# Performance work log

Measured on AMD Instinct MI355X. Metric: run time of the kernel, lower is better.

## Reference

```python
import jax, jax.numpy as jnp
import numpy as np

N, T, K, R = 192, 32, 3, 2  # nodes, timesteps, filter taps, downsampling rate


def setup_inputs() -> dict:
    key = jax.random.key(0)
    ks = jax.random.split(key, 7)
    X = jax.random.normal(ks[0], (N, T), dtype=jnp.float32)
    # scale Sg so powers of the product-graph shift stay numerically tame
    Sg = jax.random.normal(ks[1], (N, N), dtype=jnp.float32) / np.float32(np.sqrt(N))
    s = jax.random.normal(ks[2], (2, 2), dtype=jnp.float32) * 0.5
    h_e1 = jax.random.normal(ks[3], (16, 1, K), dtype=jnp.float32) * 0.3
    h_e2 = jax.random.normal(ks[4], (32, 16, K), dtype=jnp.float32) * 0.3
    h_d1 = jax.random.normal(ks[5], (16, 32, K), dtype=jnp.float32) * 0.3
    h_d2 = jax.random.normal(ks[6], (1, 16, K), dtype=jnp.float32) * 0.3
    return {"X": X, "Sg": Sg, "s": s, "h_e1": h_e1, "h_e2": h_e2,
            "h_d1": h_d1, "h_d2": h_d2}


def _temp_graph(t):
    # torch.eye(t).roll(1, dims=-1).t() : cyclic directed shift, S[(i+1)%t, i] = 1
    return jnp.roll(jnp.eye(t, dtype=jnp.float32), 1, axis=1).T


def _product_powers(St, Sg, s):
    # S = sum_{i,j in {0,1}} s[i,j] * kron(St^i, Sg^j); return stacked S^0..S^{K-1}
    t, n = St.shape[0], Sg.shape[0]
    It = jnp.eye(t, dtype=jnp.float32)
    In = jnp.eye(n, dtype=jnp.float32)
    S = (s[0, 0] * jnp.kron(It, In) + s[0, 1] * jnp.kron(It, Sg)
         + s[1, 0] * jnp.kron(St, In) + s[1, 1] * jnp.kron(St, Sg))
    powers = [jnp.eye(t * n, dtype=jnp.float32)]
    for _ in range(K - 1):
        powers.append(powers[-1] @ S)
    return jnp.stack(powers)  # (K, t*n, t*n)


def _conv(x, Sp, h):
    # GTConvLayerDense: Y[:, o] = sum_i sum_k h[o,i,k] * S^k @ x[:, i]
    xp = jnp.einsum('knm,mi->kni', Sp, x)  # (K, NT, Cin)
    return jnp.einsum('kni,oik->no', xp, h)  # (NT, Cout)


def _down(x, n, t):
    # columnvec layout: row index = time*n + node; max-pool over R consecutive times
    c = x.shape[-1]
    return x.reshape(t // R, R, n, c).max(axis=1).reshape((t // R) * n, c)


def _up(x, n, t, tt):
    # zero-stuff every R-th timestep up to target length tt
    c = x.shape[-1]
    z = jnp.zeros((tt, n, c), dtype=x.dtype)
    return z.at[::R].set(x.reshape(t, n, c)).reshape(tt * n, c)


def reference(X, Sg, s, h_e1, h_e2, h_d1, h_d2):
    n, t = X.shape
    Ts = [t, t // R, t // (R * R)]  # [32, 16, 8]
    Sp0 = _product_powers(_temp_graph(Ts[0]), Sg, s)  # (K, n*T, n*T)
    Sp1 = _product_powers(_temp_graph(Ts[1]), Sg, s)
    x = X.T.reshape(n * t, 1)  # columnvec
    # encoder: conv -> downsample(max) -> relu
    x = jax.nn.relu(_down(_conv(x, Sp0, h_e1), n, Ts[0]))
    x = jax.nn.relu(_down(_conv(x, Sp1, h_e2), n, Ts[1]))
    # decoder: upsample -> relu -> conv
    x = _conv(jax.nn.relu(_up(x, n, Ts[2], Ts[1])), Sp1, h_d1)
    x = _conv(jax.nn.relu(_up(x, n, Ts[1], Ts[0])), Sp0, h_d2)
    return x.reshape(t, n).T  # inversevec -> (N, T)
```

## Files before the change

kernel.cpp:

```cpp
#include <hip/hip_runtime.h>


#define NODES 192
typedef float4 f4;

__device__ __forceinline__ void compute_c(const float* __restrict__ s, float c[3][3][3]) {
    const float s00 = s[0], s01 = s[1], s10 = s[2], s11 = s[3];
    #pragma unroll
    for (int k = 0; k < 3; ++k)
        #pragma unroll
        for (int d = 0; d < 3; ++d)
            #pragma unroll
            for (int p = 0; p < 3; ++p) c[k][d][p] = 0.f;
    c[0][0][0] = 1.f;
    c[1][0][0] = s00; c[1][0][1] = s01;
    c[1][1][0] = s10; c[1][1][1] = s11;
    c[2][0][0] = s00 * s00;       c[2][0][1] = 2.f * s00 * s01;               c[2][0][2] = s01 * s01;
    c[2][1][0] = 2.f * s00 * s10; c[2][1][1] = 2.f * (s00 * s11 + s01 * s10); c[2][1][2] = 2.f * s11 * s01;
    c[2][2][0] = s10 * s10;       c[2][2][1] = 2.f * s10 * s11;               c[2][2][2] = s11 * s11;
}

__global__ __launch_bounds__(768) void prep_kernel(
        const float* __restrict__ X, const float* __restrict__ Sg, const float* __restrict__ s,
        const float* __restrict__ he1, const float* __restrict__ he2,
        const float* __restrict__ hd1, const float* __restrict__ hd2,
        float* __restrict__ ws) {
    const int b = blockIdx.x, tid = threadIdx.x;
    float* SgTp  = ws;
    float* Sg2Tp = ws + 36864;
    float* XT    = ws + 73728;
    float* G     = ws + 79872;
    if (b < 192) {
        __shared__ float row[NODES];
        __shared__ float ps[4 * NODES];
        if (tid < NODES) {
            const float v = Sg[b * NODES + tid];
            row[tid] = v;
            SgTp[(tid >> 2) * 768 + b * 4 + (tid & 3)] = v;
        }
        __syncthreads();
        const int n = tid % NODES, q = tid / NODES;
        float v[48];
        #pragma unroll
        for (int rr = 0; rr < 48; ++rr) v[rr] = Sg[(48 * q + rr) * NODES + n];
        float acc = 0.f;
        #pragma unroll
        for (int rr = 0; rr < 48; ++rr) acc += row[48 * q + rr] * v[rr];
        ps[q * NODES + n] = acc;
        __syncthreads();
        if (q == 0) {
            const float s2 = ps[n] + ps[NODES + n] + ps[2 * NODES + n] + ps[3 * NODES + n];
            Sg2Tp[(n >> 2) * 768 + b * 4 + (n & 3)] = s2;
        }
    } else if (b == 192) {
        float c[3][3][3];
        compute_c(s, c);
        for (int w = tid; w < 1056; w += 768) {
            const float* h; int gbase, pl;
            if (w < 16)        { h = he1; gbase = 0;     pl = w; }
            else if (w < 528)  { h = he2; gbase = 192;   pl = w - 16; }
            else if (w < 1040) { h = hd1; gbase = 6336;  pl = w - 528; }
            else               { h = hd2; gbase = 12480; pl = w - 1040; }
            const float h0 = h[pl * 3], h1 = h[pl * 3 + 1], h2 = h[pl * 3 + 2];
            float* gp = G + gbase + pl * 12;
            #pragma unroll
            for (int dp = 0; dp < 12; ++dp) {
                float val = 0.f;
                if (dp < 9) { const int d = dp / 3, p = dp % 3;
                              val = h0 * c[0][d][p] + h1 * c[1][d][p] + h2 * c[2][d][p]; }
                gp[dp] = val;
            }
        }
    } else {
        if (tid < NODES) {
            const f4* xr = (const f4*)(X + tid * 32);
            f4 vv[8];
            #pragma unroll
            for (int qq = 0; qq < 8; ++qq) vv[qq] = xr[qq];
            #pragma unroll
            for (int qq = 0; qq < 8; ++qq) {
                XT[(4 * qq + 0) * NODES + tid] = vv[qq].x;
                XT[(4 * qq + 1) * NODES + tid] = vv[qq].y;
                XT[(4 * qq + 2) * NODES + tid] = vv[qq].z;
                XT[(4 * qq + 3) * NODES + tid] = vv[qq].w;
            }
        }
    }
}

template <int CIN, int TREAL, int INMODE, int UP>
__global__ __launch_bounds__(768) void zkern(
        const float* __restrict__ src, const f4* __restrict__ Ap, const f4* __restrict__ Bp,
        float* __restrict__ Z1, float* __restrict__ Z2) {
    const int t = blockIdx.x % TREAL, i = blockIdx.x / TREAL;
    const int m = threadIdx.x % NODES, q = threadIdx.x / NODES;
    __shared__ __align__(16) float xs[NODES];
    __shared__ float ps[8 * NODES];
    if (threadIdx.x < NODES) {
        float v = (INMODE == 0) ? src[t * NODES + threadIdx.x]
                                : src[(t * CIN + i) * NODES + threadIdx.x];
        if (INMODE == 2) v = fmaxf(v, 0.f);
        xs[threadIdx.x] = v;
    }
    __syncthreads();
    f4 va[12], vb[12];
    #pragma unroll
    for (int jj = 0; jj < 12; ++jj) va[jj] = Ap[(12 * q + jj) * NODES + m];
    #pragma unroll
    for (int jj = 0; jj < 12; ++jj) vb[jj] = Bp[(12 * q + jj) * NODES + m];
    const f4* xv = (const f4*)xs;
    float a1 = 0.f, a2 = 0.f;
    #pragma unroll
    for (int jj = 0; jj < 12; ++jj) {
        const f4 x = xv[12 * q + jj];
        a1 += va[jj].x * x.x + va[jj].y * x.y + va[jj].z * x.z + va[jj].w * x.w;
        a2 += vb[jj].x * x.x + vb[jj].y * x.y + vb[jj].z * x.z + vb[jj].w * x.w;
    }
    ps[q * NODES + m] = a1;
    ps[(4 + q) * NODES + m] = a2;
    __syncthreads();
    const int t2 = UP ? 2 * t : t;
    const int base = (t2 * CIN + i) * NODES + m;
    if (q == 0)
        Z1[base] = ps[m] + ps[NODES + m] + ps[2 * NODES + m] + ps[3 * NODES + m];
    else if (q == 1)
        Z2[base] = ps[4 * NODES + m] + ps[5 * NODES + m] + ps[6 * NODES + m] + ps[7 * NODES + m];
    else if (UP && q == 2)
        Z1[((t2 + 1) * CIN + i) * NODES + m] = 0.f;
    else if (UP && q == 3)
        Z2[((t2 + 1) * CIN + i) * NODES + m] = 0.f;
}

__global__ __launch_bounds__(768) void f1_ker(
        const float* __restrict__ XT, const float* __restrict__ Zx1, const float* __restrict__ Zx2,
        const float* __restrict__ ge1, float* __restrict__ B1) {
    const int q = blockIdx.x;
    const int m = threadIdx.x % NODES, og = threadIdx.x / NODES;
    __shared__ __align__(16) float gls[192];
    if (threadIdx.x < 192) gls[threadIdx.x] = ge1[threadIdx.x];
    float x0[4], z1[4], z2[4];
    #pragma unroll
    for (int dl = 0; dl < 4; ++dl) {
        const int u = (2 * q + dl - 2) & 31;
        x0[dl] = XT[u * NODES + m];
        z1[dl] = Zx1[u * NODES + m];
        z2[dl] = Zx2[u * NODES + m];
    }
    __syncthreads();
    #pragma unroll
    for (int oi = 0; oi < 4; ++oi) {
        const int o = og * 4 + oi;
        const float* gr = &gls[o * 12];
        const f4 ga = *(const f4*)gr, gb = *(const f4*)(gr + 4), gc = *(const f4*)(gr + 8);
        float a[2];
        #pragma unroll
        for (int tt = 0; tt < 2; ++tt)
            a[tt] = ga.x * x0[tt + 2] + ga.y * z1[tt + 2] + ga.z * z2[tt + 2]
                  + ga.w * x0[tt + 1] + gb.x * z1[tt + 1] + gb.y * z2[tt + 1]
                  + gb.z * x0[tt]     + gb.w * z1[tt]     + gc.x * z2[tt];
        B1[(q * 16 + o) * NODES + m] = fmaxf(fmaxf(a[0], a[1]), 0.f);
    }
}

__global__ __launch_bounds__(768) void f2_ker(
        const float* __restrict__ B1,
        const float* __restrict__ ZB1, const float* __restrict__ ZB2,
        const float* __restrict__ ge2, float* __restrict__ B2) {
    const int q = blockIdx.x & 7, oo = blockIdx.x >> 3;
    const int m = threadIdx.x % NODES, cq = threadIdx.x / NODES;
    __shared__ __align__(16) float gls[1536];
    __shared__ float ps[4 * 2 * 8 * NODES];
    for (int idx = threadIdx.x; idx < 1536; idx += 768) gls[idx] = ge2[oo * 1536 + idx];
    const int i0 = cq * 4;
    float xv[4][4], z1v[4][4], z2v[4][4];
    #pragma unroll
    for (int dl = 0; dl < 4; ++dl) {
        const int u = (2 * q + dl - 2) & 15;
        const int base = (u * 16 + i0) * NODES + m;
        #pragma unroll
        for (int ii = 0; ii < 4; ++ii) xv[dl][ii]  = B1[base + ii * NODES];
        #pragma unroll
        for (int ii = 0; ii < 4; ++ii) z1v[dl][ii] = ZB1[base + ii * NODES];
        #pragma unroll
        for (int ii = 0; ii < 4; ++ii) z2v[dl][ii] = ZB2[base + ii * NODES];
    }
    __syncthreads();
    #pragma unroll
    for (int o = 0; o < 8; ++o) {
        float a[2] = {0.f, 0.f};
        #pragma unroll
        for (int ii = 0; ii < 4; ++ii) {
            const float* gr = &gls[(o * 16 + i0 + ii) * 12];
            const f4 ga = *(const f4*)gr, gb = *(const f4*)(gr + 4), gc = *(const f4*)(gr + 8);
            #pragma unroll
            for (int tt = 0; tt < 2; ++tt)
                a[tt] += ga.x * xv[tt + 2][ii] + ga.y * z1v[tt + 2][ii] + ga.z * z2v[tt + 2][ii]
                       + ga.w * xv[tt + 1][ii] + gb.x * z1v[tt + 1][ii] + gb.y * z2v[tt + 1][ii]
                       + gb.z * xv[tt][ii]     + gb.w * z1v[tt][ii]     + gc.x * z2v[tt][ii];
        }
        ps[((cq * 2 + 0) * 8 + o) * NODES + m] = a[0];
        ps[((cq * 2 + 1) * 8 + o) * NODES + m] = a[1];
    }
    __syncthreads();
    #pragma unroll
    for (int oi = 0; oi < 2; ++oi) {
        const int o = cq * 2 + oi;
        float r0 = 0.f, r1 = 0.f;
        #pragma unroll
        for (int c = 0; c < 4; ++c) {
            r0 += ps[((c * 2 + 0) * 8 + o) * NODES + m];
            r1 += ps[((c * 2 + 1) * 8 + o) * NODES + m];
        }
        B2[(q * 32 + oo * 8 + o) * NODES + m] = fmaxf(fmaxf(r0, r1), 0.f);
    }
}

__global__ __launch_bounds__(768) void f3_ker(
        const float* __restrict__ B2,
        const float* __restrict__ ZA1, const float* __restrict__ ZA2,
        const float* __restrict__ gd1, float* __restrict__ B3) {
    const int t = blockIdx.x & 15, og = blockIdx.x >> 4;
    const int m = threadIdx.x % NODES, cq = threadIdx.x / NODES;
    __shared__ __align__(16) float gls[1536];
    __shared__ float ps[4 * 4 * NODES];
    for (int idx = threadIdx.x; idx < 1536; idx += 768) gls[idx] = gd1[og * 1536 + idx];
    float acc[4] = {0.f, 0.f, 0.f, 0.f};
    #pragma unroll
    for (int cc = 0; cc < 2; ++cc) {
        const int i0 = cq * 8 + cc * 4;
        float xv[3][4], z1v[3][4], z2v[3][4];
        #pragma unroll
        for (int dl = 0; dl < 3; ++dl) {
            const int u = (t + dl - 2) & 15;
            const float msk = (u & 1) ? 0.f : 1.f;
            const int sb = ((u >> 1) * 32 + i0) * NODES + m;
            const int zb = (u * 32 + i0) * NODES + m;
            #pragma unroll
            for (int ii = 0; ii < 4; ++ii) xv[dl][ii]  = B2[sb + ii * NODES] * msk;
            #pragma unroll
            for (int ii = 0; ii < 4; ++ii) z1v[dl][ii] = ZA1[zb + ii * NODES];
            #pragma unroll
            for (int ii = 0; ii < 4; ++ii) z2v[dl][ii] = ZA2[zb + ii * NODES];
        }
        if (cc == 0) __syncthreads();
        #pragma unroll
        for (int o = 0; o < 4; ++o)
            #pragma unroll
            for (int ii = 0; ii < 4; ++ii) {
                const float* gr = &gls[(o * 32 + i0 + ii) * 12];
                const f4 ga = *(const f4*)gr, gb = *(const f4*)(gr + 4), gc = *(const f4*)(gr + 8);
                acc[o] += ga.x * xv[2][ii] + ga.y * z1v[2][ii] + ga.z * z2v[2][ii]
                        + ga.w * xv[1][ii] + gb.x * z1v[1][ii] + gb.y * z2v[1][ii]
                        + gb.z * xv[0][ii] + gb.w * z1v[0][ii] + gc.x * z2v[0][ii];
            }
    }
    #pragma unroll
    for (int o = 0; o < 4; ++o) ps[(cq * 4 + o) * NODES + m] = acc[o];
    __syncthreads();
    {
        const int o = cq;
        const float raw = ps[(0 * 4 + o) * NODES + m] + ps[(1 * 4 + o) * NODES + m]
                        + ps[(2 * 4 + o) * NODES + m] + ps[(3 * 4 + o) * NODES + m];
        B3[(t * 16 + og * 4 + o) * NODES + m] = raw;
    }
}

__global__ __launch_bounds__(768) void f4_ker(
        const float* __restrict__ B3,
        const float* __restrict__ ZC1, const float* __restrict__ ZC2,
        const float* __restrict__ gd2, float* __restrict__ out) {
    const int t = blockIdx.x;
    const int m = threadIdx.x % NODES, cq = threadIdx.x / NODES;
    __shared__ __align__(16) float gls[192];
    __shared__ float ps[4 * NODES];
    if (threadIdx.x < 192) gls[threadIdx.x] = gd2[threadIdx.x];
    const int i0 = cq * 4;
    float xv[3][4], z1v[3][4], z2v[3][4];
    #pragma unroll
    for (int dl = 0; dl < 3; ++dl) {
        const int u = (t + dl - 2) & 31;
        const float msk = (u & 1) ? 0.f : 1.f;
        const int sb = ((u >> 1) * 16 + i0) * NODES + m;
        const int zb = (u * 16 + i0) * NODES + m;
        #pragma unroll
        for (int ii = 0; ii < 4; ++ii) xv[dl][ii]  = fmaxf(B3[sb + ii * NODES], 0.f) * msk;
        #pragma unroll
        for (int ii = 0; ii < 4; ++ii) z1v[dl][ii] = ZC1[zb + ii * NODES];
        #pragma unroll
        for (int ii = 0; ii < 4; ++ii) z2v[dl][ii] = ZC2[zb + ii * NODES];
    }
    __syncthreads();
    float acc = 0.f;
    #pragma unroll
    for (int ii = 0; ii < 4; ++ii) {
        const float* gr = &gls[(i0 + ii) * 12];
        const f4 ga = *(const f4*)gr, gb = *(const f4*)(gr + 4), gc = *(const f4*)(gr + 8);
        acc += ga.x * xv[2][ii] + ga.y * z1v[2][ii] + ga.z * z2v[2][ii]
             + ga.w * xv[1][ii] + gb.x * z1v[1][ii] + gb.y * z2v[1][ii]
             + gb.z * xv[0][ii] + gb.w * z1v[0][ii] + gc.x * z2v[0][ii];
    }
    ps[cq * NODES + m] = acc;
    __syncthreads();
    if (cq == 0)
        out[m * 32 + t] = ps[m] + ps[NODES + m] + ps[2 * NODES + m] + ps[3 * NODES + m];
}

extern "C" void kernel_launch(void* const* d_in, const int* in_sizes, int n_in,
                              void* d_out, int out_size, void* d_ws, size_t ws_size,
                              hipStream_t stream) {
    (void)in_sizes; (void)n_in; (void)out_size; (void)ws_size;
    const float* X   = (const float*)d_in[0];
    const float* Sg  = (const float*)d_in[1];
    const float* s   = (const float*)d_in[2];
    const float* he1 = (const float*)d_in[3];
    const float* he2 = (const float*)d_in[4];
    const float* hd1 = (const float*)d_in[5];
    const float* hd2 = (const float*)d_in[6];
    float* out = (float*)d_out;
    float* ws  = (float*)d_ws;

    const f4* Ap = (const f4*)(ws);
    const f4* Bp = (const f4*)(ws + 36864);
    float* XT  = ws + 73728;
    float* GE1 = ws + 79872;
    float* GE2 = ws + 80064;
    float* GD1 = ws + 86208;
    float* GD2 = ws + 92352;
    float* Zx1 = ws + 92544;
    float* Zx2 = ws + 98688;
    float* ZB1 = ws + 104832;
    float* ZB2 = ws + 153984;
    float* ZA1 = ws + 203136;
    float* ZA2 = ws + 301440;
    float* ZC1 = ws + 399744;
    float* ZC2 = ws + 498048;
    float* B1  = ws + 596352;
    float* B2  = ws + 645504;
    float* B3  = ws + 694656;

    prep_kernel<<<194, 768, 0, stream>>>(X, Sg, s, he1, he2, hd1, hd2, ws);
    zkern<1, 32, 0, 0><<<32, 768, 0, stream>>>(XT, Ap, Bp, Zx1, Zx2);
    f1_ker<<<16, 768, 0, stream>>>(XT, Zx1, Zx2, GE1, B1);
    zkern<16, 16, 1, 0><<<256, 768, 0, stream>>>(B1, Ap, Bp, ZB1, ZB2);
    f2_ker<<<32, 768, 0, stream>>>(B1, ZB1, ZB2, GE2, B2);
    zkern<32, 8, 1, 1><<<256, 768, 0, stream>>>(B2, Ap, Bp, ZA1, ZA2);
    f3_ker<<<64, 768, 0, stream>>>(B2, ZA1, ZA2, GD1, B3);
    zkern<16, 16, 2, 1><<<256, 768, 0, stream>>>(B3, Ap, Bp, ZC1, ZC2);
    f4_ker<<<32, 768, 0, stream>>>(B3, ZC1, ZC2, GD2, out);
}
```

Before: 103.3 us.

## Fuse all stages into one persistent kernel with software grid barriers

Replaces the nine separate launches (prep, four z-projection kernels, four filter kernels) with a single 192-block persistent kernel. Stages are separated by atomic-counter grid barriers, and each filter stage is fused with the following Sg/Sg² projection through shared memory. This removes launch overhead and several global round-trips of intermediates. In exchange it relies on all 192 blocks of 768 threads being co-resident, since the spin barrier deadlocks otherwise, and it adds a reset handshake on the barrier counters at every call.

New measurement: 288.8 us. 2.8x slower.

```diff
diff --git a/kernel.cpp b/kernel.cpp
--- a/kernel.cpp
+++ b/kernel.cpp
@@ -2,6 +2,7 @@
 
 
 #define NODES 192
+#define NBLK 192
 typedef float4 f4;
 
 __device__ __forceinline__ void compute_c(const float* __restrict__ s, float c[3][3][3]) {
@@ -20,289 +21,422 @@
     c[2][2][0] = s10 * s10;       c[2][2][1] = 2.f * s10 * s11;               c[2][2][2] = s11 * s11;
 }
 
-__global__ __launch_bounds__(768) void prep_kernel(
+__device__ __forceinline__ void gridbar(unsigned* cell) {
+    __syncthreads();
+    if (threadIdx.x == 0) {
+        __threadfence();
+        const unsigned got = atomicAdd(cell, 1u) + 1u;
+        if (got != (unsigned)NBLK) {
+            while (__hip_atomic_load(cell, __ATOMIC_RELAXED, __HIP_MEMORY_SCOPE_AGENT)
+                   != (unsigned)NBLK)
+                __builtin_amdgcn_s_sleep(8);
+        }
+    }
+    __syncthreads();
+    __threadfence();
+}
+
+__global__ __launch_bounds__(768) void mono_kernel(
         const float* __restrict__ X, const float* __restrict__ Sg, const float* __restrict__ s,
         const float* __restrict__ he1, const float* __restrict__ he2,
         const float* __restrict__ hd1, const float* __restrict__ hd2,
-        float* __restrict__ ws) {
+        float* __restrict__ out, float* __restrict__ ws) {
     const int b = blockIdx.x, tid = threadIdx.x;
+    const int m = tid % NODES, q = tid / NODES;
+
     float* SgTp  = ws;
     float* Sg2Tp = ws + 36864;
     float* XT    = ws + 73728;
     float* G     = ws + 79872;
-    if (b < 192) {
-        __shared__ float row[NODES];
-        __shared__ float ps[4 * NODES];
+    float* GE1 = G, *GE2 = G + 192, *GD1 = G + 6336, *GD2 = G + 12480;
+    float* ZB1 = ws + 104832, *ZB2 = ws + 153984;
+    float* ZA1 = ws + 203136, *ZA2 = ws + 301440;
+    float* ZC1 = ws + 399744, *ZC2 = ws + 498048;
+    float* B1  = ws + 596352, *B2 = ws + 645504, *B3 = ws + 694656;
+    unsigned* bars = (unsigned*)(ws + 743808);
+    const f4* Ap = (const f4*)SgTp;
+    const f4* Bp = (const f4*)Sg2Tp;
+
+    __shared__ __align__(16) float sm_x[4 * NODES];
+    __shared__ __align__(16) float sm_v[4 * NODES];
+    __shared__ __align__(16) float sm_zx1[4 * NODES];
+    __shared__ __align__(16) float sm_zx2[4 * NODES];
+    __shared__ __align__(16) float sm_g[1536];
+    __shared__ __align__(16) float sm_ps[6144];
+
+    if (tid == 0) {
+        if (b == 0) {
+            for (int k = 0; k < 5; ++k) atomicExch(&bars[k * 32], 0u);
+            __threadfence();
+            atomicExch(&bars[5 * 32], 0x900DBEEFu);
+        } else {
+            while (__hip_atomic_load(&bars[5 * 32], __ATOMIC_RELAXED, __HIP_MEMORY_SCOPE_AGENT)
+                   != 0x900DBEEFu)
+                __builtin_amdgcn_s_sleep(8);
+        }
+    }
+    __syncthreads();
+    __threadfence();
+
+    {
         if (tid < NODES) {
             const float v = Sg[b * NODES + tid];
-            row[tid] = v;
+            sm_x[tid] = v;
             SgTp[(tid >> 2) * 768 + b * 4 + (tid & 3)] = v;
         }
         __syncthreads();
-        const int n = tid % NODES, q = tid / NODES;
-        float v[48];
-        #pragma unroll
-        for (int rr = 0; rr < 48; ++rr) v[rr] = Sg[(48 * q + rr) * NODES + n];
-        float acc = 0.f;
-        #pragma unroll
-        for (int rr = 0; rr < 48; ++rr) acc += row[48 * q + rr] * v[rr];
-        ps[q * NODES + n] = acc;
+        {
+            float v[48];
+            #pragma unroll
+            for (int rr = 0; rr < 48; ++rr) v[rr] = Sg[(48 * q + rr) * NODES + m];
+            float acc = 0.f;
+            #pragma unroll
+            for (int rr = 0; rr < 48; ++rr) acc += sm_x[48 * q + rr] * v[rr];
+            sm_ps[q * NODES + m] = acc;
+        }
         __syncthreads();
         if (q == 0) {
-            const float s2 = ps[n] + ps[NODES + n] + ps[2 * NODES + n] + ps[3 * NODES + n];
-            Sg2Tp[(n >> 2) * 768 + b * 4 + (n & 3)] = s2;
-        }
-    } else if (b == 192) {
-        float c[3][3][3];
-        compute_c(s, c);
-        for (int w = tid; w < 1056; w += 768) {
-            const float* h; int gbase, pl;
-            if (w < 16)        { h = he1; gbase = 0;     pl = w; }
-            else if (w < 528)  { h = he2; gbase = 192;   pl = w - 16; }
-            else if (w < 1040) { h = hd1; gbase = 6336;  pl = w - 528; }
-            else               { h = hd2; gbase = 12480; pl = w - 1040; }
-            const float h0 = h[pl * 3], h1 = h[pl * 3 + 1], h2 = h[pl * 3 + 2];
-            float* gp = G + gbase + pl * 12;
-            #pragma unroll
-            for (int dp = 0; dp < 12; ++dp) {
+            const float s2 = sm_ps[m] + sm_ps[NODES + m] + sm_ps[2 * NODES + m] + sm_ps[3 * NODES + m];
+            Sg2Tp[(m >> 2) * 768 + b * 4 + (m & 3)] = s2;
+        }
+        if (b == 0) {
+            float c[3][3][3];
+            compute_c(s, c);
+            for (int w = tid; w < 1056; w += 768) {
+                const float* hh; int gbase, pl;
+                if (w < 16)        { hh = he1; gbase = 0;     pl = w; }
+                else if (w < 528)  { hh = he2; gbase = 192;   pl = w - 16; }
+                else if (w < 1040) { hh = hd1; gbase = 6336;  pl = w - 528; }
+                else               { hh = hd2; gbase = 12480; pl = w - 1040; }
+                const float h0 = hh[pl * 3], h1 = hh[pl * 3 + 1], h2 = hh[pl * 3 + 2];
+                float* gp = G + gbase + pl * 12;
+                #pragma unroll
+                for (int dp = 0; dp < 12; ++dp) {
+                    float val = 0.f;
+                    if (dp < 9) { const int d = dp / 3, p = dp % 3;
+                                  val = h0 * c[0][d][p] + h1 * c[1][d][p] + h2 * c[2][d][p]; }
+                    gp[dp] = val;
+                }
+            }
+        } else if (b == 1) {
+            if (tid < NODES) {
+                const f4* xr = (const f4*)(X + tid * 32);
+                f4 vv[8];
+                #pragma unroll
+                for (int qq = 0; qq < 8; ++qq) vv[qq] = xr[qq];
+                #pragma unroll
+                for (int qq = 0; qq < 8; ++qq) {
+                    XT[(4 * qq + 0) * NODES + tid] = vv[qq].x;
+                    XT[(4 * qq + 1) * NODES + tid] = vv[qq].y;
+                    XT[(4 * qq + 2) * NODES + tid] = vv[qq].z;
+                    XT[(4 * qq + 3) * NODES + tid] = vv[qq].w;
+                }
+            }
+        }
+    }
+    gridbar(&bars[0]);
+
+    if (b < 64) {
+        const int tq = b & 15, o0 = (b >> 4) * 4;
+        {
+            const int u = (2 * tq + q - 2) & 31;
+            sm_x[q * NODES + m] = XT[u * NODES + m];
+        }
+        if (tid < 48) sm_g[tid] = GE1[o0 * 12 + tid];
+        __syncthreads();
+        {
+            f4 va[12], vb[12];
+            #pragma unroll
+            for (int j = 0; j < 12; ++j) va[j] = Ap[(12 * q + j) * NODES + m];
+            #pragma unroll
+            for (int j = 0; j < 12; ++j) vb[j] = Bp[(12 * q + j) * NODES + m];
+            #pragma unroll
+            for (int ch = 0; ch < 4; ++ch) {
+                const f4* xr = (const f4*)(sm_x + ch * NODES);
+                float a1 = 0.f, a2 = 0.f;
+                #pragma unroll
+                for (int j = 0; j < 12; ++j) {
+                    const f4 x = xr[12 * q + j];
+                    a1 += va[j].x * x.x + va[j].y * x.y + va[j].z * x.z + va[j].w * x.w;
+                    a2 += vb[j].x * x.x + vb[j].y * x.y + vb[j].z * x.z + vb[j].w * x.w;
+                }
+                sm_ps[((0 * 4 + ch) * 4 + q) * NODES + m] = a1;
+                sm_ps[((1 * 4 + ch) * 4 + q) * NODES + m] = a2;
+            }
+        }
+        __syncthreads();
+        {
+            #pragma unroll
+            for (int pp = 0; pp < 2; ++pp) {
+                const int pi = q * 2 + pp, mat = pi >> 2, ch = pi & 3;
                 float val = 0.f;
-                if (dp < 9) { const int d = dp / 3, p = dp % 3;
-                              val = h0 * c[0][d][p] + h1 * c[1][d][p] + h2 * c[2][d][p]; }
-                gp[dp] = val;
-            }
-        }
-    } else {
-        if (tid < NODES) {
-            const f4* xr = (const f4*)(X + tid * 32);
-            f4 vv[8];
-            #pragma unroll
-            for (int qq = 0; qq < 8; ++qq) vv[qq] = xr[qq];
-            #pragma unroll
-            for (int qq = 0; qq < 8; ++qq) {
-                XT[(4 * qq + 0) * NODES + tid] = vv[qq].x;
-                XT[(4 * qq + 1) * NODES + tid] = vv[qq].y;
-                XT[(4 * qq + 2) * NODES + tid] = vv[qq].z;
-                XT[(4 * qq + 3) * NODES + tid] = vv[qq].w;
-            }
-        }
-    }
-}
-
-template <int CIN, int TREAL, int INMODE, int UP>
-__global__ __launch_bounds__(768) void zkern(
-        const float* __restrict__ src, const f4* __restrict__ Ap, const f4* __restrict__ Bp,
-        float* __restrict__ Z1, float* __restrict__ Z2) {
-    const int t = blockIdx.x % TREAL, i = blockIdx.x / TREAL;
-    const int m = threadIdx.x % NODES, q = threadIdx.x / NODES;
-    __shared__ __align__(16) float xs[NODES];
-    __shared__ float ps[8 * NODES];
-    if (threadIdx.x < NODES) {
-        float v = (INMODE == 0) ? src[t * NODES + threadIdx.x]
-                                : src[(t * CIN + i) * NODES + threadIdx.x];
-        if (INMODE == 2) v = fmaxf(v, 0.f);
-        xs[threadIdx.x] = v;
-    }
-    __syncthreads();
-    f4 va[12], vb[12];
-    #pragma unroll
-    for (int jj = 0; jj < 12; ++jj) va[jj] = Ap[(12 * q + jj) * NODES + m];
-    #pragma unroll
-    for (int jj = 0; jj < 12; ++jj) vb[jj] = Bp[(12 * q + jj) * NODES + m];
-    const f4* xv = (const f4*)xs;
-    float a1 = 0.f, a2 = 0.f;
-    #pragma unroll
-    for (int jj = 0; jj < 12; ++jj) {
-        const f4 x = xv[12 * q + jj];
-        a1 += va[jj].x * x.x + va[jj].y * x.y + va[jj].z * x.z + va[jj].w * x.w;
-        a2 += vb[jj].x * x.x + vb[jj].y * x.y + vb[jj].z * x.z + vb[jj].w * x.w;
-    }
-    ps[q * NODES + m] = a1;
-    ps[(4 + q) * NODES + m] = a2;
-    __syncthreads();
-    const int t2 = UP ? 2 * t : t;
-    const int base = (t2 * CIN + i) * NODES + m;
-    if (q == 0)
-        Z1[base] = ps[m] + ps[NODES + m] + ps[2 * NODES + m] + ps[3 * NODES + m];
-    else if (q == 1)
-        Z2[base] = ps[4 * NODES + m] + ps[5 * NODES + m] + ps[6 * NODES + m] + ps[7 * NODES + m];
-    else if (UP && q == 2)
-        Z1[((t2 + 1) * CIN + i) * NODES + m] = 0.f;
-    else if (UP && q == 3)
-        Z2[((t2 + 1) * CIN + i) * NODES + m] = 0.f;
-}
-
-__global__ __launch_bounds__(768) void f1_ker(
-        const float* __restrict__ XT, const float* __restrict__ Zx1, const float* __restrict__ Zx2,
-        const float* __restrict__ ge1, float* __restrict__ B1) {
-    const int q = blockIdx.x;
-    const int m = threadIdx.x % NODES, og = threadIdx.x / NODES;
-    __shared__ __align__(16) float gls[192];
-    if (threadIdx.x < 192) gls[threadIdx.x] = ge1[threadIdx.x];
-    float x0[4], z1[4], z2[4];
-    #pragma unroll
-    for (int dl = 0; dl < 4; ++dl) {
-        const int u = (2 * q + dl - 2) & 31;
-        x0[dl] = XT[u * NODES + m];
-        z1[dl] = Zx1[u * NODES + m];
-        z2[dl] = Zx2[u * NODES + m];
-    }
-    __syncthreads();
-    #pragma unroll
-    for (int oi = 0; oi < 4; ++oi) {
-        const int o = og * 4 + oi;
-        const float* gr = &gls[o * 12];
-        const f4 ga = *(const f4*)gr, gb = *(const f4*)(gr + 4), gc = *(const f4*)(gr + 8);
-        float a[2];
-        #pragma unroll
-        for (int tt = 0; tt < 2; ++tt)
-            a[tt] = ga.x * x0[tt + 2] + ga.y * z1[tt + 2] + ga.z * z2[tt + 2]
-                  + ga.w * x0[tt + 1] + gb.x * z1[tt + 1] + gb.y * z2[tt + 1]
-                  + gb.z * x0[tt]     + gb.w * z1[tt]     + gc.x * z2[tt];
-        B1[(q * 16 + o) * NODES + m] = fmaxf(fmaxf(a[0], a[1]), 0.f);
-    }
-}
-
-__global__ __launch_bounds__(768) void f2_ker(
-        const float* __restrict__ B1,
-        const float* __restrict__ ZB1, const float* __restrict__ ZB2,
-        const float* __restrict__ ge2, float* __restrict__ B2) {
-    const int q = blockIdx.x & 7, oo = blockIdx.x >> 3;
-    const int m = threadIdx.x % NODES, cq = threadIdx.x / NODES;
-    __shared__ __align__(16) float gls[1536];
-    __shared__ float ps[4 * 2 * 8 * NODES];
-    for (int idx = threadIdx.x; idx < 1536; idx += 768) gls[idx] = ge2[oo * 1536 + idx];
-    const int i0 = cq * 4;
-    float xv[4][4], z1v[4][4], z2v[4][4];
-    #pragma unroll
-    for (int dl = 0; dl < 4; ++dl) {
-        const int u = (2 * q + dl - 2) & 15;
-        const int base = (u * 16 + i0) * NODES + m;
-        #pragma unroll
-        for (int ii = 0; ii < 4; ++ii) xv[dl][ii]  = B1[base + ii * NODES];
-        #pragma unroll
-        for (int ii = 0; ii < 4; ++ii) z1v[dl][ii] = ZB1[base + ii * NODES];
-        #pragma unroll
-        for (int ii = 0; ii < 4; ++ii) z2v[dl][ii] = ZB2[base + ii * NODES];
-    }
-    __syncthreads();
-    #pragma unroll
-    for (int o = 0; o < 8; ++o) {
-        float a[2] = {0.f, 0.f};
-        #pragma unroll
-        for (int ii = 0; ii < 4; ++ii) {
-            const float* gr = &gls[(o * 16 + i0 + ii) * 12];
+                #pragma unroll
+                for (int qq = 0; qq < 4; ++qq)
+                    val += sm_ps[((mat * 4 + ch) * 4 + qq) * NODES + m];
+                (mat == 0 ? sm_zx1 : sm_zx2)[ch * NODES + m] = val;
+            }
+        }
+        __syncthreads();
+        {
+            float x0[4], z1[4], z2[4];
+            #pragma unroll
+            for (int dl = 0; dl < 4; ++dl) {
+                x0[dl] = sm_x[dl * NODES + m];
+                z1[dl] = sm_zx1[dl * NODES + m];
+                z2[dl] = sm_zx2[dl * NODES + m];
+            }
+            const float* gr = &sm_g[q * 12];
             const f4 ga = *(const f4*)gr, gb = *(const f4*)(gr + 4), gc = *(const f4*)(gr + 8);
+            float a[2];
             #pragma unroll
             for (int tt = 0; tt < 2; ++tt)
-                a[tt] += ga.x * xv[tt + 2][ii] + ga.y * z1v[tt + 2][ii] + ga.z * z2v[tt + 2][ii]
-                       + ga.w * xv[tt + 1][ii] + gb.x * z1v[tt + 1][ii] + gb.y * z2v[tt + 1][ii]
-                       + gb.z * xv[tt][ii]     + gb.w * z1v[tt][ii]     + gc.x * z2v[tt][ii];
-        }
-        ps[((cq * 2 + 0) * 8 + o) * NODES + m] = a[0];
-        ps[((cq * 2 + 1) * 8 + o) * NODES + m] = a[1];
-    }
-    __syncthreads();
-    #pragma unroll
-    for (int oi = 0; oi < 2; ++oi) {
-        const int o = cq * 2 + oi;
-        float r0 = 0.f, r1 = 0.f;
-        #pragma unroll
-        for (int c = 0; c < 4; ++c) {
-            r0 += ps[((c * 2 + 0) * 8 + o) * NODES + m];
-            r1 += ps[((c * 2 + 1) * 8 + o) * NODES + m];
-        }
-        B2[(q * 32 + oo * 8 + o) * NODES + m] = fmaxf(fmaxf(r0, r1), 0.f);
-    }
-}
-
-__global__ __launch_bounds__(768) void f3_ker(
-        const float* __restrict__ B2,
-        const float* __restrict__ ZA1, const float* __restrict__ ZA2,
-        const float* __restrict__ gd1, float* __restrict__ B3) {
-    const int t = blockIdx.x & 15, og = blockIdx.x >> 4;
-    const int m = threadIdx.x % NODES, cq = threadIdx.x / NODES;
-    __shared__ __align__(16) float gls[1536];
-    __shared__ float ps[4 * 4 * NODES];
-    for (int idx = threadIdx.x; idx < 1536; idx += 768) gls[idx] = gd1[og * 1536 + idx];
-    float acc[4] = {0.f, 0.f, 0.f, 0.f};
-    #pragma unroll
-    for (int cc = 0; cc < 2; ++cc) {
-        const int i0 = cq * 8 + cc * 4;
-        float xv[3][4], z1v[3][4], z2v[3][4];
-        #pragma unroll
-        for (int dl = 0; dl < 3; ++dl) {
-            const int u = (t + dl - 2) & 15;
-            const float msk = (u & 1) ? 0.f : 1.f;
-            const int sb = ((u >> 1) * 32 + i0) * NODES + m;
-            const int zb = (u * 32 + i0) * NODES + m;
-            #pragma unroll
-            for (int ii = 0; ii < 4; ++ii) xv[dl][ii]  = B2[sb + ii * NODES] * msk;
-            #pragma unroll
-            for (int ii = 0; ii < 4; ++ii) z1v[dl][ii] = ZA1[zb + ii * NODES];
-            #pragma unroll
-            for (int ii = 0; ii < 4; ++ii) z2v[dl][ii] = ZA2[zb + ii * NODES];
-        }
-        if (cc == 0) __syncthreads();
-        #pragma unroll
-        for (int o = 0; o < 4; ++o)
+                a[tt] = ga.x * x0[tt + 2] + ga.y * z1[tt + 2] + ga.z * z2[tt + 2]
+                      + ga.w * x0[tt + 1] + gb.x * z1[tt + 1] + gb.y * z2[tt + 1]
+                      + gb.z * x0[tt]     + gb.w * z1[tt]     + gc.x * z2[tt];
+            const float v = fmaxf(fmaxf(a[0], a[1]), 0.f);
+            B1[(tq * 16 + o0 + q) * NODES + m] = v;
+            sm_v[q * NODES + m] = v;
+        }
+        __syncthreads();
+        {
+            f4 va[12], vb[12];
+            #pragma unroll
+            for (int j = 0; j < 12; ++j) va[j] = Ap[(12 * q + j) * NODES + m];
+            #pragma unroll
+            for (int j = 0; j < 12; ++j) vb[j] = Bp[(12 * q + j) * NODES + m];
+            #pragma unroll
+            for (int ch = 0; ch < 4; ++ch) {
+                const f4* xr = (const f4*)(sm_v + ch * NODES);
+                float a1 = 0.f, a2 = 0.f;
+                #pragma unroll
+                for (int j = 0; j < 12; ++j) {
+                    const f4 x = xr[12 * q + j];
+                    a1 += va[j].x * x.x + va[j].y * x.y + va[j].z * x.z + va[j].w * x.w;
+                    a2 += vb[j].x * x.x + vb[j].y * x.y + vb[j].z * x.z + vb[j].w * x.w;
+                }
+                sm_ps[((0 * 4 + ch) * 4 + q) * NODES + m] = a1;
+                sm_ps[((1 * 4 + ch) * 4 + q) * NODES + m] = a2;
+            }
+        }
+        __syncthreads();
+        {
+            #pragma unroll
+            for (int pp = 0; pp < 2; ++pp) {
+                const int pi = q * 2 + pp, mat = pi >> 2, ch = pi & 3;
+                float val = 0.f;
+                #pragma unroll
+                for (int qq = 0; qq < 4; ++qq)
+                    val += sm_ps[((mat * 4 + ch) * 4 + qq) * NODES + m];
+                (mat == 0 ? ZB1 : ZB2)[(tq * 16 + o0 + ch) * NODES + m] = val;
+            }
+        }
+    }
+    gridbar(&bars[1 * 32]);
+
+    if (b < 64) {
+        const int q8 = b & 7, o0 = (b >> 3) * 4;
+        for (int idx = tid; idx < 768; idx += 768) sm_g[idx] = GE2[(o0 * 16) * 12 + idx];
+        {
+            const int i0 = q * 4;
+            float xv[4][4], z1v[4][4], z2v[4][4];
+            #pragma unroll
+            for (int dl = 0; dl < 4; ++dl) {
+                const int u = (2 * q8 + dl - 2) & 15;
+                const int base = (u * 16 + i0) * NODES + m;
+                #pragma unroll
+                for (int ii = 0; ii < 4; ++ii) xv[dl][ii]  = B1[base + ii * NODES];
+                #pragma unroll
+                for (int ii = 0; ii < 4; ++ii) z1v[dl][ii] = ZB1[base + ii * NODES];
+                #pragma unroll
+                for (int ii = 0; ii < 4; ++ii) z2v[dl][ii] = ZB2[base + ii * NODES];
+            }
+            __syncthreads();
+            #pragma unroll
+            for (int o = 0; o < 4; ++o) {
+                float a[2] = {0.f, 0.f};
+                #pragma unroll
+                for (int ii = 0; ii < 4; ++ii) {
+                    const float* gr = &sm_g[(o * 16 + i0 + ii) * 12];
+                    const f4 ga = *(const f4*)gr, gb = *(const f4*)(gr + 4), gc = *(const f4*)(gr + 8);
+                    #pragma unroll
+                    for (int tt = 0; tt < 2; ++tt)
+                        a[tt] += ga.x * xv[tt + 2][ii] + ga.y * z1v[tt + 2][ii] + ga.z * z2v[tt + 2][ii]
+                               + ga.w * xv[tt + 1][ii] + gb.x * z1v[tt + 1][ii] + gb.y * z2v[tt + 1][ii]
+                               + gb.z * xv[tt][ii]     + gb.w * z1v[tt][ii]     + gc.x * z2v[tt][ii];
+                }
+                sm_ps[((q * 4 + o) * 2 + 0) * NODES + m] = a[0];
+                sm_ps[((q * 4 + o) * 2 + 1) * NODES + m] = a[1];
+            }
+        }
+        __syncthreads();
+        {
+            float r0 = 0.f, r1 = 0.f;
+            #pragma unroll
+            for (int cq = 0; cq < 4; ++cq) {
+                r0 += sm_ps[((cq * 4 + q) * 2 + 0) * NODES + m];
+                r1 += sm_ps[((cq * 4 + q) * 2 + 1) * NODES + m];
+            }
+            const float v = fmaxf(fmaxf(r0, r1), 0.f);
+            B2[(q8 * 32 + o0 + q) * NODES + m] = v;
+            sm_v[q * NODES + m] = v;
+        }
+        __syncthreads();
+        {
+            f4 va[12], vb[12];
+            #pragma unroll
+            for (int j = 0; j < 12; ++j) va[j] = Ap[(12 * q + j) * NODES + m];
+            #pragma unroll
+            for (int j = 0; j < 12; ++j) vb[j] = Bp[(12 * q + j) * NODES + m];
+            #pragma unroll
+            for (int ch = 0; ch < 4; ++ch) {
+                const f4* xr = (const f4*)(sm_v + ch * NODES);
+                float a1 = 0.f, a2 = 0.f;
+                #pragma unroll
+                for (int j = 0; j < 12; ++j) {
+                    const f4 x = xr[12 * q + j];
+                    a1 += va[j].x * x.x + va[j].y * x.y + va[j].z * x.z + va[j].w * x.w;
+                    a2 += vb[j].x * x.x + vb[j].y * x.y + vb[j].z * x.z + vb[j].w * x.w;
+                }
+                sm_ps[((0 * 4 + ch) * 4 + q) * NODES + m] = a1;
+                sm_ps[((1 * 4 + ch) * 4 + q) * NODES + m] = a2;
+            }
+        }
+        __syncthreads();
+        {
+            const int t2 = 2 * q8;
+            #pragma unroll
+            for (int pp = 0; pp < 2; ++pp) {
+                const int pi = q * 2 + pp, mat = pi >> 2, ch = pi & 3;
+                float val = 0.f;
+                #pragma unroll
+                for (int qq = 0; qq < 4; ++qq)
+                    val += sm_ps[((mat * 4 + ch) * 4 + qq) * NODES + m];
+                float* Z = (mat == 0) ? ZA1 : ZA2;
+                Z[(t2 * 32 + o0 + ch) * NODES + m] = val;
+                Z[((t2 + 1) * 32 + o0 + ch) * NODES + m] = 0.f;
+            }
+        }
+    }
+    gridbar(&bars[2 * 32]);
+
+    if (b < 64) {
+        const int t16 = b & 15, o0 = (b >> 4) * 4;
+        for (int idx = tid; idx < 1536; idx += 768) sm_g[idx] = GD1[(o0 * 32) * 12 + idx];
+        __syncthreads();
+        {
+            float acc[4] = {0.f, 0.f, 0.f, 0.f};
+            #pragma unroll
+            for (int cc = 0; cc < 2; ++cc) {
+                const int i0 = cc * 16 + q * 4;
+                float xv[3][4], z1v[3][4], z2v[3][4];
+                #pragma unroll
+                for (int dl = 0; dl < 3; ++dl) {
+                    const int u = (t16 + dl - 2) & 15;
+                    const float msk = (u & 1) ? 0.f : 1.f;
+                    const int sb = ((u >> 1) * 32 + i0) * NODES + m;
+                    const int zb = (u * 32 + i0) * NODES + m;
+                    #pragma unroll
+                    for (int ii = 0; ii < 4; ++ii) xv[dl][ii]  = B2[sb + ii * NODES] * msk;
+                    #pragma unroll
+                    for (int ii = 0; ii < 4; ++ii) z1v[dl][ii] = ZA1[zb + ii * NODES];
+                    #pragma unroll
+                    for (int ii = 0; ii < 4; ++ii) z2v[dl][ii] = ZA2[zb + ii * NODES];
+                }
+                #pragma unroll
+                for (int o = 0; o < 4; ++o)
+                    #pragma unroll
+                    for (int ii = 0; ii < 4; ++ii) {
+                        const float* gr = &sm_g[(o * 32 + i0 + ii) * 12];
+                        const f4 ga = *(const f4*)gr, gb = *(const f4*)(gr + 4), gc = *(const f4*)(gr + 8);
+                        acc[o] += ga.x * xv[2][ii] + ga.y * z1v[2][ii] + ga.z * z2v[2][ii]
+                                + ga.w * xv[1][ii] + gb.x * z1v[1][ii] + gb.y * z2v[1][ii]
+                                + gb.z * xv[0][ii] + gb.w * z1v[0][ii] + gc.x * z2v[0][ii];
+                    }
+            }
+            #pragma unroll
+            for (int o = 0; o < 4; ++o) sm_ps[(q * 4 + o) * NODES + m] = acc[o];
+        }
+        __syncthreads();
+        {
+            const float raw = sm_ps[(0 * 4 + q) * NODES + m] + sm_ps[(1 * 4 + q) * NODES + m]
+                            + sm_ps[(2 * 4 + q) * NODES + m] + sm_ps[(3 * 4 + q) * NODES + m];
+            B3[(t16 * 16 + o0 + q) * NODES + m] = raw;
+            sm_v[q * NODES + m] = fmaxf(raw, 0.f);
+        }
+        __syncthreads();
+        {
+            f4 va[12], vb[12];
+            #pragma unroll
+            for (int j = 0; j < 12; ++j) va[j] = Ap[(12 * q + j) * NODES + m];
+            #pragma unroll
+            for (int j = 0; j < 12; ++j) vb[j] = Bp[(12 * q + j) * NODES + m];
+            #pragma unroll
+            for (int ch = 0; ch < 4; ++ch) {
+                const f4* xr = (const f4*)(sm_v + ch * NODES);
+                float a1 = 0.f, a2 = 0.f;
+                #pragma unroll
+                for (int j = 0; j < 12; ++j) {
+                    const f4 x = xr[12 * q + j];
+                    a1 += va[j].x * x.x + va[j].y * x.y + va[j].z * x.z + va[j].w * x.w;
+                    a2 += vb[j].x * x.x + vb[j].y * x.y + vb[j].z * x.z + vb[j].w * x.w;
+                }
+                sm_ps[((0 * 4 + ch) * 4 + q) * NODES + m] = a1;
+                sm_ps[((1 * 4 + ch) * 4 + q) * NODES + m] = a2;
+            }
+        }
+        __syncthreads();
+        {
+            const int t2 = 2 * t16;
+            #pragma unroll
+            for (int pp = 0; pp < 2; ++pp) {
+                const int pi = q * 2 + pp, mat = pi >> 2, ch = pi & 3;
+                float val = 0.f;
+                #pragma unroll
+                for (int qq = 0; qq < 4; ++qq)
+                    val += sm_ps[((mat * 4 + ch) * 4 + qq) * NODES + m];
+                float* Z = (mat == 0) ? ZC1 : ZC2;
+                Z[(t2 * 16 + o0 + ch) * NODES + m] = val;
+                Z[((t2 + 1) * 16 + o0 + ch) * NODES + m] = 0.f;
+            }
+        }
+    }
+    gridbar(&bars[3 * 32]);
+
+    if (b < 32) {
+        const int t = b;
+        if (tid < 192) sm_g[tid] = GD2[tid];
+        {
+            const int i0 = q * 4;
+            float xv[3][4], z1v[3][4], z2v[3][4];
+            #pragma unroll
+            for (int dl = 0; dl < 3; ++dl) {
+                const int u = (t + dl - 2) & 31;
+                const float msk = (u & 1) ? 0.f : 1.f;
+                const int sb = ((u >> 1) * 16 + i0) * NODES + m;
+                const int zb = (u * 16 + i0) * NODES + m;
+                #pragma unroll
+                for (int ii = 0; ii < 4; ++ii) xv[dl][ii]  = fmaxf(B3[sb + ii * NODES], 0.f) * msk;
+                #pragma unroll
+                for (int ii = 0; ii < 4; ++ii) z1v[dl][ii] = ZC1[zb + ii * NODES];
+                #pragma unroll
+                for (int ii = 0; ii < 4; ++ii) z2v[dl][ii] = ZC2[zb + ii * NODES];
+            }
+            __syncthreads();
+            float acc = 0.f;
             #pragma unroll
             for (int ii = 0; ii < 4; ++ii) {
-                const float* gr = &gls[(o * 32 + i0 + ii) * 12];
+                const float* gr = &sm_g[(i0 + ii) * 12];
                 const f4 ga = *(const f4*)gr, gb = *(const f4*)(gr + 4), gc = *(const f4*)(gr + 8);
-                acc[o] += ga.x * xv[2][ii] + ga.y * z1v[2][ii] + ga.z * z2v[2][ii]
-                        + ga.w * xv[1][ii] + gb.x * z1v[1][ii] + gb.y * z2v[1][ii]
-                        + gb.z * xv[0][ii] + gb.w * z1v[0][ii] + gc.x * z2v[0][ii];
-            }
-    }
-    #pragma unroll
-    for (int o = 0; o < 4; ++o) ps[(cq * 4 + o) * NODES + m] = acc[o];
-    __syncthreads();
-    {
-        const int o = cq;
-        const float raw = ps[(0 * 4 + o) * NODES + m] + ps[(1 * 4 + o) * NODES + m]
-                        + ps[(2 * 4 + o) * NODES + m] + ps[(3 * 4 + o) * NODES + m];
-        B3[(t * 16 + og * 4 + o) * NODES + m] = raw;
-    }
-}
-
-__global__ __launch_bounds__(768) void f4_ker(
-        const float* __restrict__ B3,
-        const float* __restrict__ ZC1, const float* __restrict__ ZC2,
-        const float* __restrict__ gd2, float* __restrict__ out) {
-    const int t = blockIdx.x;
-    const int m = threadIdx.x % NODES, cq = threadIdx.x / NODES;
-    __shared__ __align__(16) float gls[192];
-    __shared__ float ps[4 * NODES];
-    if (threadIdx.x < 192) gls[threadIdx.x] = gd2[threadIdx.x];
-    const int i0 = cq * 4;
-    float xv[3][4], z1v[3][4], z2v[3][4];
-    #pragma unroll
-    for (int dl = 0; dl < 3; ++dl) {
-        const int u = (t + dl - 2) & 31;
-        const float msk = (u & 1) ? 0.f : 1.f;
-        const int sb = ((u >> 1) * 16 + i0) * NODES + m;
-        const int zb = (u * 16 + i0) * NODES + m;
-        #pragma unroll
-        for (int ii = 0; ii < 4; ++ii) xv[dl][ii]  = fmaxf(B3[sb + ii * NODES], 0.f) * msk;
-        #pragma unroll
-        for (int ii = 0; ii < 4; ++ii) z1v[dl][ii] = ZC1[zb + ii * NODES];
-        #pragma unroll
-        for (int ii = 0; ii < 4; ++ii) z2v[dl][ii] = ZC2[zb + ii * NODES];
-    }
-    __syncthreads();
-    float acc = 0.f;
-    #pragma unroll
-    for (int ii = 0; ii < 4; ++ii) {
-        const float* gr = &gls[(i0 + ii) * 12];
-        const f4 ga = *(const f4*)gr, gb = *(const f4*)(gr + 4), gc = *(const f4*)(gr + 8);
-        acc += ga.x * xv[2][ii] + ga.y * z1v[2][ii] + ga.z * z2v[2][ii]
-             + ga.w * xv[1][ii] + gb.x * z1v[1][ii] + gb.y * z2v[1][ii]
-             + gb.z * xv[0][ii] + gb.w * z1v[0][ii] + gc.x * z2v[0][ii];
-    }
-    ps[cq * NODES + m] = acc;
-    __syncthreads();
-    if (cq == 0)
-        out[m * 32 + t] = ps[m] + ps[NODES + m] + ps[2 * NODES + m] + ps[3 * NODES + m];
+                acc += ga.x * xv[2][ii] + ga.y * z1v[2][ii] + ga.z * z2v[2][ii]
+                     + ga.w * xv[1][ii] + gb.x * z1v[1][ii] + gb.y * z2v[1][ii]
+                     + gb.z * xv[0][ii] + gb.w * z1v[0][ii] + gc.x * z2v[0][ii];
+            }
+            sm_ps[q * NODES + m] = acc;
+        }
+        __syncthreads();
+        if (q == 0)
+            out[m * 32 + t] = sm_ps[m] + sm_ps[NODES + m] + sm_ps[2 * NODES + m] + sm_ps[3 * NODES + m];
+    }
 }
 
 extern "C" void kernel_launch(void* const* d_in, const int* in_sizes, int n_in,
@@ -316,35 +450,6 @@
     const float* he2 = (const float*)d_in[4];
     const float* hd1 = (const float*)d_in[5];
     const float* hd2 = (const float*)d_in[6];
-    float* out = (float*)d_out;
-    float* ws  = (float*)d_ws;
-
-    const f4* Ap = (const f4*)(ws);
-    const f4* Bp = (const f4*)(ws + 36864);
-    float* XT  = ws + 73728;
-    float* GE1 = ws + 79872;
-    float* GE2 = ws + 80064;
-    float* GD1 = ws + 86208;
-    float* GD2 = ws + 92352;
-    float* Zx1 = ws + 92544;
-    float* Zx2 = ws + 98688;
-    float* ZB1 = ws + 104832;
-    float* ZB2 = ws + 153984;
-    float* ZA1 = ws + 203136;
-    float* ZA2 = ws + 301440;
-    float* ZC1 = ws + 399744;
-    float* ZC2 = ws + 498048;
-    float* B1  = ws + 596352;
-    float* B2  = ws + 645504;
-    float* B3  = ws + 694656;
-
-    prep_kernel<<<194, 768, 0, stream>>>(X, Sg, s, he1, he2, hd1, hd2, ws);
-    zkern<1, 32, 0, 0><<<32, 768, 0, stream>>>(XT, Ap, Bp, Zx1, Zx2);
-    f1_ker<<<16, 768, 0, stream>>>(XT, Zx1, Zx2, GE1, B1);
-    zkern<16, 16, 1, 0><<<256, 768, 0, stream>>>(B1, Ap, Bp, ZB1, ZB2);
-    f2_ker<<<32, 768, 0, stream>>>(B1, ZB1, ZB2, GE2, B2);
-    zkern<32, 8, 1, 1><<<256, 768, 0, stream>>>(B2, Ap, Bp, ZA1, ZA2);
-    f3_ker<<<64, 768, 0, stream>>>(B2, ZA1, ZA2, GD1, B3);
-    zkern<16, 16, 2, 1><<<256, 768, 0, stream>>>(B3, Ap, Bp, ZC1, ZC2);
-    f4_ker<<<32, 768, 0, stream>>>(B3, ZC1, ZC2, GD2, out);
+    mono_kernel<<<NBLK, 768, 0, stream>>>(X, Sg, s, he1, he2, hd1, hd2,
+                                          (float*)d_out, (float*)d_ws);
 }
```
